# Kernel tuning notes

Hardware: AMD Instinct MI355X
Metric: run time of the kernel (lower is better)

The kernel has to match this reference:

```python
import jax, jax.numpy as jnp
import numpy as np

H = 128
W = 128
DELTA = 7000.0  # sigmainv in the original (delta default 7000)


def setup_inputs() -> dict:
    key = jax.random.key(0)
    k1, k2, k3, k4 = jax.random.split(key, 4)
    B, P, F, TH, TW = 2, 300, 512, 512, 512
    points_bxpx3 = jax.random.uniform(k1, (B, P, 3), jnp.float32) * 2.0 - 1.0  # NDC cube [-1,1]
    faces_fx3 = jax.random.randint(k2, (F, 3), 0, P, dtype=jnp.int32)
    uv_bxpx2 = jax.random.uniform(k3, (B, P, 2), jnp.float32)  # texcoords in [0,1]
    texture_bx3xthxtw = jax.random.uniform(k4, (B, 3, TH, TW), jnp.float32)
    return {"points_bxpx3": points_bxpx3, "faces_fx3": faces_fx3,
            "uv_bxpx2": uv_bxpx2, "texture_bx3xthxtw": texture_bx3xthxtw}


def _edge(ax, ay, bx, by, px, py):
    # signed area * 2 of triangle (a, b, p); standard edge function
    return (bx - ax) * (py - ay) - (by - ay) * (px - ax)


def _seg_d2(ax, ay, bx, by, px, py):
    # squared distance from point p to segment (a, b)
    abx, aby = bx - ax, by - ay
    apx, apy = px - ax, py - ay
    denom = abx * abx + aby * aby + 1e-12
    t = jnp.clip((apx * abx + apy * aby) / denom, 0.0, 1.0)
    dx = apx - t * abx
    dy = apy - t * aby
    return dx * dx + dy * dy


def _rasterize(points_bxpx3, faces_fx3, feats_bxfx3xd, height, width, delta):
    """Soft DIB-R-style rasterizer.
    Returns (imfeat [B,H,W,D], improb [B,H,W,1]).
    """
    B = points_bxpx3.shape[0]
    v = points_bxpx3[:, faces_fx3]                      # (B,F,3,3) gathered face vertices
    x0, x1, x2 = (v[:, :, i, 0][:, :, None, None] for i in range(3))
    y0, y1, y2 = (v[:, :, i, 1][:, :, None, None] for i in range(3))
    z0, z1, z2 = (v[:, :, i, 2][:, :, None, None] for i in range(3))

    # pixel-center grid in NDC; y flipped (top row = +1)
    px = ((jnp.arange(width, dtype=points_bxpx3.dtype) + 0.5) / width * 2.0 - 1.0)[None, None, None, :]
    py = (1.0 - (jnp.arange(height, dtype=points_bxpx3.dtype) + 0.5) / height * 2.0)[None, None, :, None]

    area = _edge(x0, y0, x1, y1, x2, y2)                # (B,F,1,1) == normal_z (cross-product z)
    front = area > 1e-8                                  # front-facing (normalz > 0) cull
    inv_area = 1.0 / jnp.where(front, area, 1.0)

    w0 = _edge(x1, y1, x2, y2, px, py) * inv_area        # (B,F,H,W) barycentrics
    w1 = _edge(x2, y2, x0, y0, px, py) * inv_area
    w2 = _edge(x0, y0, x1, y1, px, py) * inv_area
    inside = front & (w0 >= 0) & (w1 >= 0) & (w2 >= 0)

    z_pix = w0 * z0 + w1 * z1 + w2 * z2                  # interpolated depth
    zbuf = jnp.where(inside, z_pix, -1e9)
    best = jnp.argmax(zbuf, axis=1)                      # (B,H,W) nearest covering face
    hit = jnp.any(inside, axis=1)[..., None].astype(points_bxpx3.dtype)  # (B,H,W,1)

    # gather winning barycentrics and per-face vertex features
    w = jnp.stack([w0, w1, w2], axis=-1)                 # (B,F,H,W,3)
    idx = jnp.broadcast_to(best[:, None, :, :, None], (B, 1, height, width, 3))
    wb = jnp.take_along_axis(w, idx, axis=1)[:, 0]       # (B,H,W,3)
    fb = jax.vmap(lambda f, i: f[i])(feats_bxfx3xd, best)  # (B,H,W,3,D)
    imfeat = jnp.einsum('bhwk,bhwkd->bhwd', wb, fb) * hit

    # soft coverage: prob of each face = exp(-delta * d2(pixel, triangle)); z-buffer blend
    d2 = jnp.minimum(
        jnp.minimum(_seg_d2(x0, y0, x1, y1, px, py), _seg_d2(x1, y1, x2, y2, px, py)),
        _seg_d2(x2, y2, x0, y0, px, py))
    d2 = jnp.where(inside, 0.0, d2)
    p = jnp.where(front, jnp.exp(-delta * d2), 0.0)      # (B,F,H,W)
    log_miss = jnp.sum(jnp.log1p(-jnp.clip(p, 0.0, 1.0 - 1e-7)), axis=1)  # (B,H,W)
    improb = (1.0 - jnp.exp(log_miss))[..., None]
    return imfeat, improb


def _fragmentshader(imtexcoords, texture_bx3xthxtw, hardmask):
    # bilinear texture sampling; background is zero
    B, C, TH, TW = texture_bx3xthxtw.shape
    u = jnp.clip(imtexcoords[..., 0], 0.0, 1.0)
    vv = jnp.clip(imtexcoords[..., 1], 0.0, 1.0)
    fx = u * (TW - 1)
    fy = (1.0 - vv) * (TH - 1)
    x0 = jnp.floor(fx).astype(jnp.int32); x1 = jnp.minimum(x0 + 1, TW - 1)
    y0 = jnp.floor(fy).astype(jnp.int32); y1 = jnp.minimum(y0 + 1, TH - 1)
    wx = (fx - x0)[:, None]; wy = (fy - y0)[:, None]     # (B,1,H,W)

    def g(tex, yy, xx):  # tex (C,TH,TW), yy/xx (H,W) -> (C,H,W)
        return tex[:, yy, xx]
    c00 = jax.vmap(g)(texture_bx3xthxtw, y0, x0)
    c01 = jax.vmap(g)(texture_bx3xthxtw, y0, x1)
    c10 = jax.vmap(g)(texture_bx3xthxtw, y1, x0)
    c11 = jax.vmap(g)(texture_bx3xthxtw, y1, x1)
    col = (c00 * (1 - wx) * (1 - wy) + c01 * wx * (1 - wy)
           + c10 * (1 - wx) * wy + c11 * wx * wy)        # (B,C,H,W)
    return col.transpose(0, 2, 3, 1) * hardmask          # (B,H,W,C)


def reference(points_bxpx3, faces_fx3, uv_bxpx2, texture_bx3xthxtw):
    # texture mode: per-face vertex features = [u, v, mask=1]
    uvf = uv_bxpx2[:, faces_fx3]                          # (B,F,3,2)
    ones = jnp.ones_like(uvf[..., :1])
    feats = jnp.concatenate([uvf, ones], axis=-1)         # (B,F,3,3)
    imfeat, improb = _rasterize(points_bxpx3, faces_fx3, feats, H, W, DELTA)
    imtexcoords = imfeat[..., :2]
    hardmask = jax.lax.stop_gradient(imfeat[..., 2:3])    # .detach() in the original
    imrender = _fragmentshader(imtexcoords, texture_bx3xthxtw, hardmask)
    return imrender, improb
```

## Files before the change

### kernel.cpp

```cpp
#include <hip/hip_runtime.h>
#include <math.h>

constexpr int kB = 2, kP = 300, kF = 512, kH = 128, kW = 128, kTH = 512, kTW = 512;
constexpr float kDelta = 7000.0f;
constexpr float kCut = 0.0363f;
constexpr float kThr2 = 0.012928f;
constexpr float kLogInside = -15.9423847f;

__global__ __launch_bounds__(512, 6) void render_all(const float* __restrict__ pts,
                                                     const int* __restrict__ faces,
                                                     const float* __restrict__ uvs,
                                                     const float* __restrict__ tex,
                                                     float* __restrict__ out) {
    __shared__ float4 sA[kF], sB[kF], sC[kF];
    __shared__ float2 s_vtx[kF * 3];
    __shared__ ushort4 s_j3[kF];
    __shared__ float s_uv[kP * 2];
    __shared__ float s_bz[512];
    __shared__ int s_bi[512];
    __shared__ float s_lm[512];
    __shared__ float4 s_pxW[64];
    __shared__ int4 s_pxO[64];
    __shared__ int s_wsum[8];

    int tile = (int)blockIdx.x;
    int b = tile >> 8;
    int rem = tile & 255;
    int ty = rem >> 4, tx = rem & 15;
    int tid = (int)threadIdx.x;
    int lane = tid & 63;
    int wv = tid >> 6;

    {
        int f = tid;
        int i0 = faces[f * 3 + 0], i1 = faces[f * 3 + 1], i2 = faces[f * 3 + 2];
        const float* pb = pts + b * kP * 3;
        float x0 = pb[i0 * 3], y0 = pb[i0 * 3 + 1], z0 = pb[i0 * 3 + 2];
        float x1 = pb[i1 * 3], y1 = pb[i1 * 3 + 1], z1 = pb[i1 * 3 + 2];
        float x2 = pb[i2 * 3], y2 = pb[i2 * 3 + 1], z2 = pb[i2 * 3 + 2];
        float area = (x1 - x0) * (y2 - y0) - (y1 - y0) * (x2 - x0);
        bool front = area > 1e-8f;

        const float* gu = uvs + b * (kP * 2);
        for (int i = tid; i < kP * 2; i += 512) s_uv[i] = gu[i];
        sA[f] = make_float4(0.0f, 0.0f, -1e30f, 0.0f);
        sB[f] = make_float4(0.0f, -1e30f, 0.0f, 0.0f);
        sC[f] = make_float4(-1e30f, 0.0f, 0.0f, 0.0f);
        s_vtx[f * 3 + 0] = make_float2(1e15f, 1e15f);
        s_vtx[f * 3 + 1] = make_float2(1e15f, 1e15f);
        s_vtx[f * 3 + 2] = make_float2(1e15f, 1e15f);
        unsigned long long bal = __ballot(front);
        if (lane == 0) s_wsum[wv] = __popcll(bal);
        __syncthreads();

        int base = 0;
#pragma unroll
        for (int w = 0; w < 8; ++w) base += (w < wv) ? s_wsum[w] : 0;
        int k = base + __popcll(bal & ((1ull << lane) - 1ull));

        if (front) {
            int slot = ((k & 7) << 6) | (k >> 3);
            float inv_a = 1.0f / area;
            float e0x = x2 - x1, e0y = y2 - y1;
            float e1x = x0 - x2, e1y = y0 - y2;
            float e2x = x1 - x0, e2y = y1 - y0;
            float l0 = fmaf(e0x, e0x, e0y * e0y);
            float l1 = fmaf(e1x, e1x, e1y * e1y);
            float l2 = fmaf(e2x, e2x, e2y * e2y);
            float s0 = rsqrtf(l0 + 1e-12f);
            float s1 = rsqrtf(l1 + 1e-12f);
            float s2 = rsqrtf(l2 + 1e-12f);
            float A0 = -e0y * s0, B0 = e0x * s0, C0 = (e0y * x1 - e0x * y1) * s0;
            float A1 = -e1y * s1, B1 = e1x * s1, C1 = (e1y * x2 - e1x * y2) * s1;
            float A2 = -e2y * s2, B2 = e2x * s2, C2 = (e2y * x0 - e2x * y0) * s2;
            float a0 = -e0y * inv_a, b0 = e0x * inv_a, c0 = (e0y * x1 - e0x * y1) * inv_a;
            float a1 = -e1y * inv_a, b1 = e1x * inv_a, c1 = (e1y * x2 - e1x * y2) * inv_a;
            float a2 = -e2y * inv_a, b2 = e2x * inv_a, c2 = (e2y * x0 - e2x * y0) * inv_a;
            sA[slot] = make_float4(A0, B0, C0, A1);
            sB[slot] = make_float4(B1, C1, A2, B2);
            sC[slot] = make_float4(C2,
                                   a0 * z0 + a1 * z1 + a2 * z2,
                                   b0 * z0 + b1 * z1 + b2 * z2,
                                   c0 * z0 + c1 * z1 + c2 * z2);
            s_vtx[slot * 3 + 0] = make_float2(x0, y0);
            s_vtx[slot * 3 + 1] = make_float2(x1, y1);
            s_vtx[slot * 3 + 2] = make_float2(x2, y2);
            s_j3[slot] = make_ushort4((unsigned short)i0, (unsigned short)i1,
                                      (unsigned short)i2, 0);
        }
    }
    __syncthreads();

    int pyi = ty * 8 + (lane >> 3);
    int pxi = tx * 8 + (lane & 7);
    float px = ((float)pxi + 0.5f) * (2.0f / 128.0f) - 1.0f;
    float py = 1.0f - ((float)pyi + 0.5f) * (2.0f / 128.0f);

    float cx = (float)(tx * 8 + 4) * (2.0f / 128.0f) - 1.0f;
    float cy = 1.0f - (float)(ty * 8 + 4) * (2.0f / 128.0f);
    unsigned long long m;
    {
        int slt = (wv << 6) + lane;
        float4 a4 = sA[slt];
        float4 b4 = sB[slt];
        float4 c4 = sC[slt];
        float L0 = fmaf(a4.x, cx, fmaf(a4.y, cy, a4.z));
        float L1 = fmaf(a4.w, cx, fmaf(b4.x, cy, b4.y));
        float L2 = fmaf(b4.z, cx, fmaf(b4.w, cy, c4.x));
        float minc = fminf(fminf(L0, L1), L2);
        float2 v0 = s_vtx[slt * 3 + 0];
        float2 v1 = s_vtx[slt * 3 + 1];
        float2 v2 = s_vtx[slt * 3 + 2];
        float e0x = v2.x - v1.x, e0y = v2.y - v1.y;
        float e1x = v0.x - v2.x, e1y = v0.y - v2.y;
        float e2x = v1.x - v0.x, e2y = v1.y - v0.y;
        float p0x = cx - v0.x, p0y = cy - v0.y;
        float p1x = cx - v1.x, p1y = cy - v1.y;
        float p2x = cx - v2.x, p2y = cy - v2.y;
        float dot0 = fmaf(p1x, e0x, p1y * e0y), len0 = fmaf(e0x, e0x, e0y * e0y);
        float dot1 = fmaf(p2x, e1x, p2y * e1y), len1 = fmaf(e1x, e1x, e1y * e1y);
        float dot2 = fmaf(p0x, e2x, p0y * e2y), len2 = fmaf(e2x, e2x, e2y * e2y);
        float c0 = (dot0 >= 0.0f && dot0 <= len0) ? L0 * L0 : 1e30f;
        float c1 = (dot1 >= 0.0f && dot1 <= len1) ? L1 * L1 : 1e30f;
        float c2 = (dot2 >= 0.0f && dot2 <= len2) ? L2 * L2 : 1e30f;
        float dv0 = fmaf(p0x, p0x, p0y * p0y);
        float dv1 = fmaf(p1x, p1x, p1y * p1y);
        float dv2 = fmaf(p2x, p2x, p2y * p2y);
        float d2c = fminf(fminf(fminf(c0, c1), fminf(c2, dv0)), fminf(dv1, dv2));
        bool admit = (minc >= 0.0f) | (d2c <= kThr2);
        m = __ballot(admit);
    }

    float bestz = -1e9f;
    int besti = -1, icnt = 0;
    float lm = 0.0f;

    int l = -1;
    float4 h0, h1, h2;
    if (m) {
        l = (int)__builtin_ctzll(m);
        m &= (m - 1);
        int fs = (wv << 6) + l;
        h0 = sA[fs]; h1 = sB[fs]; h2 = sC[fs];
    }
    while (l >= 0) {
        int l2 = -1;
        float4 n0, n1, n2;
        if (m) {
            l2 = (int)__builtin_ctzll(m);
            m &= (m - 1);
            int fs2 = (wv << 6) + l2;
            n0 = sA[fs2]; n1 = sB[fs2]; n2 = sC[fs2];
        }
        int fs = (wv << 6) + l;
        int k = (l << 3) | wv;
        float L0 = fmaf(h0.x, px, fmaf(h0.y, py, h0.z));
        float L1 = fmaf(h0.w, px, fmaf(h1.x, py, h1.y));
        float L2 = fmaf(h1.z, px, fmaf(h1.w, py, h2.x));
        float minL = fminf(fminf(L0, L1), L2);
        bool inside = minL >= 0.0f;
        float z = fmaf(h2.y, px, fmaf(h2.z, py, h2.w));
        if (inside && z > bestz) { bestz = z; besti = k; }
        icnt += inside ? 1 : 0;
        float db = fminf(fminf(fabsf(L0), fabsf(L1)), fabsf(L2));
        bool need = (!inside) & (db < kCut);
        if (__any(need)) {
            float2 v0 = s_vtx[fs * 3 + 0];
            float2 v1 = s_vtx[fs * 3 + 1];
            float2 v2 = s_vtx[fs * 3 + 2];
            float e0x = v2.x - v1.x, e0y = v2.y - v1.y;
            float e1x = v0.x - v2.x, e1y = v0.y - v2.y;
            float e2x = v1.x - v0.x, e2y = v1.y - v0.y;
            float p0x = px - v0.x, p0y = py - v0.y;
            float p1x = px - v1.x, p1y = py - v1.y;
            float p2x = px - v2.x, p2y = py - v2.y;
            float dot0 = fmaf(p1x, e0x, p1y * e0y), len0 = fmaf(e0x, e0x, e0y * e0y);
            float dot1 = fmaf(p2x, e1x, p2y * e1y), len1 = fmaf(e1x, e1x, e1y * e1y);
            float dot2 = fmaf(p0x, e2x, p0y * e2y), len2 = fmaf(e2x, e2x, e2y * e2y);
            float c0 = (dot0 >= 0.0f && dot0 <= len0) ? L0 * L0 : 1e30f;
            float c1 = (dot1 >= 0.0f && dot1 <= len1) ? L1 * L1 : 1e30f;
            float c2 = (dot2 >= 0.0f && dot2 <= len2) ? L2 * L2 : 1e30f;
            float dv0 = fmaf(p0x, p0x, p0y * p0y);
            float dv1 = fmaf(p1x, p1x, p1y * p1y);
            float dv2 = fmaf(p2x, p2x, p2y * p2y);
            float d2 = fminf(fminf(fminf(c0, c1), fminf(c2, dv0)), fminf(dv1, dv2));
            float p = __expf(-kDelta * d2);
            p = fminf(p, 1.0f - 1e-7f);
            float lp = __logf(1.0f - p);
            lm += need ? lp : 0.0f;
        }
        l = l2; h0 = n0; h1 = n1; h2 = n2;
    }
    lm = fmaf((float)icnt, kLogInside, lm);

    s_bz[tid] = bestz;
    s_bi[tid] = besti;
    s_lm[tid] = lm;
    __syncthreads();

    if (tid < 64) {
        float bz = s_bz[tid];
        int bi = s_bi[tid];
        float L = s_lm[tid];
#pragma unroll
        for (int w = 1; w < 8; ++w) {
            float z2 = s_bz[w * 64 + tid];
            int ii = s_bi[w * 64 + tid];
            L += s_lm[w * 64 + tid];
            if (z2 > bz || (z2 == bz && ii >= 0 && (unsigned)ii < (unsigned)bi)) {
                bz = z2; bi = ii;
            }
        }
        float improb = 1.0f - expf(L);
        float u = 0.0f, v = 0.0f, mk = 0.0f;
        if (bi >= 0) {
            int slot = ((bi & 7) << 6) | (bi >> 3);
            float2 v0 = s_vtx[slot * 3 + 0];
            float2 v1 = s_vtx[slot * 3 + 1];
            float2 v2 = s_vtx[slot * 3 + 2];
            float area = (v1.x - v0.x) * (v2.y - v0.y) - (v1.y - v0.y) * (v2.x - v0.x);
            float inv_a = 1.0f / area;
            float w0 = ((v2.x - v1.x) * (py - v1.y) - (v2.y - v1.y) * (px - v1.x)) * inv_a;
            float w1 = ((v0.x - v2.x) * (py - v2.y) - (v0.y - v2.y) * (px - v2.x)) * inv_a;
            float w2 = ((v1.x - v0.x) * (py - v0.y) - (v1.y - v0.y) * (px - v0.x)) * inv_a;
            ushort4 j = s_j3[slot];
            u = w0 * s_uv[j.x * 2] + w1 * s_uv[j.y * 2] + w2 * s_uv[j.z * 2];
            v = w0 * s_uv[j.x * 2 + 1] + w1 * s_uv[j.y * 2 + 1] + w2 * s_uv[j.z * 2 + 1];
            mk = w0 + w1 + w2;
        }
        float uc = fminf(fmaxf(u, 0.0f), 1.0f);
        float vc = fminf(fmaxf(v, 0.0f), 1.0f);
        float fx = uc * (float)(kTW - 1);
        float fy = (1.0f - vc) * (float)(kTH - 1);
        int xi0 = (int)floorf(fx), yi0 = (int)floorf(fy);
        int xi1 = min(xi0 + 1, kTW - 1), yi1 = min(yi0 + 1, kTH - 1);
        float wx = fx - (float)xi0, wy = fy - (float)yi0;
        float w00 = (1.0f - wx) * (1.0f - wy) * mk;
        float w01 = wx * (1.0f - wy) * mk;
        float w10 = (1.0f - wx) * wy * mk;
        float w11 = wx * wy * mk;
        s_pxW[tid] = make_float4(w00, w01, w10, w11);
        s_pxO[tid] = make_int4(yi0 * kTW + xi0, yi0 * kTW + xi1,
                               yi1 * kTW + xi0, yi1 * kTW + xi1);
        out[kB * kH * kW * 3 + (b * kH + pyi) * kW + pxi] = improb;
    }
    __syncthreads();

    if (tid < 192) {
        int pix = tid & 63;
        int c = tid >> 6;
        float4 w = s_pxW[pix];
        int4 o = s_pxO[pix];
        const float* tc = tex + ((size_t)b * 3 + c) * kTH * kTW;
        float col = tc[o.x] * w.x + tc[o.y] * w.y + tc[o.z] * w.z + tc[o.w] * w.w;
        int qy = ty * 8 + (pix >> 3);
        int qx = tx * 8 + (pix & 7);
        out[((b * kH + qy) * kW + qx) * 3 + c] = col;
    }
}

extern "C" void kernel_launch(void* const* d_in, const int* in_sizes, int n_in,
                              void* d_out, int out_size, void* d_ws, size_t ws_size,
                              hipStream_t stream) {
    const float* pts = (const float*)d_in[0];
    const int* faces = (const int*)d_in[1];
    const float* uvs = (const float*)d_in[2];
    const float* tex = (const float*)d_in[3];
    float* out = (float*)d_out;
    render_all<<<kB * 256, 512, 0, stream>>>(pts, faces, uvs, tex, out);
}
```

Before: 18.44 us.

## Process two pixel tiles per block to amortize per-face setup

Each block now renders two adjacent 8x8 tiles in a loop, and the grid is halved, so the shared-memory face setup (gathering vertices, building edge and depth coefficients) runs once per two tiles instead of once per tile. The face loop is also simplified: the software prefetch of the next face's coefficients is dropped in favour of plain per-iteration shared loads. The tradeoff is half as many blocks in flight, which lowers parallelism across the GPU, and the two tiles run one after the other inside each block.

```diff
diff --git a/kernel.cpp b/kernel.cpp
--- a/kernel.cpp
+++ b/kernel.cpp
@@ -23,10 +23,11 @@
     __shared__ int4 s_pxO[64];
     __shared__ int s_wsum[8];
 
-    int tile = (int)blockIdx.x;
-    int b = tile >> 8;
-    int rem = tile & 255;
-    int ty = rem >> 4, tx = rem & 15;
+    int blk = (int)blockIdx.x;
+    int b = blk >> 7;
+    int rem = blk & 127;
+    int ty = rem >> 3;
+    int txp = rem & 7;
     int tid = (int)threadIdx.x;
     int lane = tid & 63;
     int wv = tid >> 6;
@@ -91,89 +92,34 @@
     }
     __syncthreads();
 
-    int pyi = ty * 8 + (lane >> 3);
-    int pxi = tx * 8 + (lane & 7);
-    float px = ((float)pxi + 0.5f) * (2.0f / 128.0f) - 1.0f;
-    float py = 1.0f - ((float)pyi + 0.5f) * (2.0f / 128.0f);
-
-    float cx = (float)(tx * 8 + 4) * (2.0f / 128.0f) - 1.0f;
-    float cy = 1.0f - (float)(ty * 8 + 4) * (2.0f / 128.0f);
-    unsigned long long m;
-    {
-        int slt = (wv << 6) + lane;
-        float4 a4 = sA[slt];
-        float4 b4 = sB[slt];
-        float4 c4 = sC[slt];
-        float L0 = fmaf(a4.x, cx, fmaf(a4.y, cy, a4.z));
-        float L1 = fmaf(a4.w, cx, fmaf(b4.x, cy, b4.y));
-        float L2 = fmaf(b4.z, cx, fmaf(b4.w, cy, c4.x));
-        float minc = fminf(fminf(L0, L1), L2);
-        float2 v0 = s_vtx[slt * 3 + 0];
-        float2 v1 = s_vtx[slt * 3 + 1];
-        float2 v2 = s_vtx[slt * 3 + 2];
-        float e0x = v2.x - v1.x, e0y = v2.y - v1.y;
-        float e1x = v0.x - v2.x, e1y = v0.y - v2.y;
-        float e2x = v1.x - v0.x, e2y = v1.y - v0.y;
-        float p0x = cx - v0.x, p0y = cy - v0.y;
-        float p1x = cx - v1.x, p1y = cy - v1.y;
-        float p2x = cx - v2.x, p2y = cy - v2.y;
-        float dot0 = fmaf(p1x, e0x, p1y * e0y), len0 = fmaf(e0x, e0x, e0y * e0y);
-        float dot1 = fmaf(p2x, e1x, p2y * e1y), len1 = fmaf(e1x, e1x, e1y * e1y);
-        float dot2 = fmaf(p0x, e2x, p0y * e2y), len2 = fmaf(e2x, e2x, e2y * e2y);
-        float c0 = (dot0 >= 0.0f && dot0 <= len0) ? L0 * L0 : 1e30f;
-        float c1 = (dot1 >= 0.0f && dot1 <= len1) ? L1 * L1 : 1e30f;
-        float c2 = (dot2 >= 0.0f && dot2 <= len2) ? L2 * L2 : 1e30f;
-        float dv0 = fmaf(p0x, p0x, p0y * p0y);
-        float dv1 = fmaf(p1x, p1x, p1y * p1y);
-        float dv2 = fmaf(p2x, p2x, p2y * p2y);
-        float d2c = fminf(fminf(fminf(c0, c1), fminf(c2, dv0)), fminf(dv1, dv2));
-        bool admit = (minc >= 0.0f) | (d2c <= kThr2);
-        m = __ballot(admit);
-    }
-
-    float bestz = -1e9f;
-    int besti = -1, icnt = 0;
-    float lm = 0.0f;
-
-    int l = -1;
-    float4 h0, h1, h2;
-    if (m) {
-        l = (int)__builtin_ctzll(m);
-        m &= (m - 1);
-        int fs = (wv << 6) + l;
-        h0 = sA[fs]; h1 = sB[fs]; h2 = sC[fs];
-    }
-    while (l >= 0) {
-        int l2 = -1;
-        float4 n0, n1, n2;
-        if (m) {
-            l2 = (int)__builtin_ctzll(m);
-            m &= (m - 1);
-            int fs2 = (wv << 6) + l2;
-            n0 = sA[fs2]; n1 = sB[fs2]; n2 = sC[fs2];
-        }
-        int fs = (wv << 6) + l;
-        int k = (l << 3) | wv;
-        float L0 = fmaf(h0.x, px, fmaf(h0.y, py, h0.z));
-        float L1 = fmaf(h0.w, px, fmaf(h1.x, py, h1.y));
-        float L2 = fmaf(h1.z, px, fmaf(h1.w, py, h2.x));
-        float minL = fminf(fminf(L0, L1), L2);
-        bool inside = minL >= 0.0f;
-        float z = fmaf(h2.y, px, fmaf(h2.z, py, h2.w));
-        if (inside && z > bestz) { bestz = z; besti = k; }
-        icnt += inside ? 1 : 0;
-        float db = fminf(fminf(fabsf(L0), fabsf(L1)), fabsf(L2));
-        bool need = (!inside) & (db < kCut);
-        if (__any(need)) {
-            float2 v0 = s_vtx[fs * 3 + 0];
-            float2 v1 = s_vtx[fs * 3 + 1];
-            float2 v2 = s_vtx[fs * 3 + 2];
+    for (int it = 0; it < 2; ++it) {
+        int tx = txp * 2 + it;
+        int pyi = ty * 8 + (lane >> 3);
+        int pxi = tx * 8 + (lane & 7);
+        float px = ((float)pxi + 0.5f) * (2.0f / 128.0f) - 1.0f;
+        float py = 1.0f - ((float)pyi + 0.5f) * (2.0f / 128.0f);
+
+        float cx = (float)(tx * 8 + 4) * (2.0f / 128.0f) - 1.0f;
+        float cy = 1.0f - (float)(ty * 8 + 4) * (2.0f / 128.0f);
+        unsigned long long m;
+        {
+            int slt = (wv << 6) + lane;
+            float4 a4 = sA[slt];
+            float4 b4 = sB[slt];
+            float4 c4 = sC[slt];
+            float L0 = fmaf(a4.x, cx, fmaf(a4.y, cy, a4.z));
+            float L1 = fmaf(a4.w, cx, fmaf(b4.x, cy, b4.y));
+            float L2 = fmaf(b4.z, cx, fmaf(b4.w, cy, c4.x));
+            float minc = fminf(fminf(L0, L1), L2);
+            float2 v0 = s_vtx[slt * 3 + 0];
+            float2 v1 = s_vtx[slt * 3 + 1];
+            float2 v2 = s_vtx[slt * 3 + 2];
             float e0x = v2.x - v1.x, e0y = v2.y - v1.y;
             float e1x = v0.x - v2.x, e1y = v0.y - v2.y;
             float e2x = v1.x - v0.x, e2y = v1.y - v0.y;
-            float p0x = px - v0.x, p0y = py - v0.y;
-            float p1x = px - v1.x, p1y = py - v1.y;
-            float p2x = px - v2.x, p2y = py - v2.y;
+            float p0x = cx - v0.x, p0y = cy - v0.y;
+            float p1x = cx - v1.x, p1y = cy - v1.y;
+            float p2x = cx - v2.x, p2y = cy - v2.y;
             float dot0 = fmaf(p1x, e0x, p1y * e0y), len0 = fmaf(e0x, e0x, e0y * e0y);
             float dot1 = fmaf(p2x, e1x, p2y * e1y), len1 = fmaf(e1x, e1x, e1y * e1y);
             float dot2 = fmaf(p0x, e2x, p0y * e2y), len2 = fmaf(e2x, e2x, e2y * e2y);
@@ -183,79 +129,125 @@
             float dv0 = fmaf(p0x, p0x, p0y * p0y);
             float dv1 = fmaf(p1x, p1x, p1y * p1y);
             float dv2 = fmaf(p2x, p2x, p2y * p2y);
-            float d2 = fminf(fminf(fminf(c0, c1), fminf(c2, dv0)), fminf(dv1, dv2));
-            float p = __expf(-kDelta * d2);
-            p = fminf(p, 1.0f - 1e-7f);
-            float lp = __logf(1.0f - p);
-            lm += need ? lp : 0.0f;
-        }
-        l = l2; h0 = n0; h1 = n1; h2 = n2;
-    }
-    lm = fmaf((float)icnt, kLogInside, lm);
-
-    s_bz[tid] = bestz;
-    s_bi[tid] = besti;
-    s_lm[tid] = lm;
-    __syncthreads();
-
-    if (tid < 64) {
-        float bz = s_bz[tid];
-        int bi = s_bi[tid];
-        float L = s_lm[tid];
+            float d2c = fminf(fminf(fminf(c0, c1), fminf(c2, dv0)), fminf(dv1, dv2));
+            bool admit = (minc >= 0.0f) | (d2c <= kThr2);
+            m = __ballot(admit);
+        }
+
+        float bestz = -1e9f;
+        int besti = -1, icnt = 0;
+        float lm = 0.0f;
+
+        while (m) {
+            int l = (int)__builtin_ctzll(m);
+            m &= (m - 1);
+            int fs = (wv << 6) + l;
+            int k = (l << 3) | wv;
+            float4 h0 = sA[fs];
+            float4 h1 = sB[fs];
+            float4 h2 = sC[fs];
+            float L0 = fmaf(h0.x, px, fmaf(h0.y, py, h0.z));
+            float L1 = fmaf(h0.w, px, fmaf(h1.x, py, h1.y));
+            float L2 = fmaf(h1.z, px, fmaf(h1.w, py, h2.x));
+            float minL = fminf(fminf(L0, L1), L2);
+            bool inside = minL >= 0.0f;
+            float z = fmaf(h2.y, px, fmaf(h2.z, py, h2.w));
+            if (inside && z > bestz) { bestz = z; besti = k; }
+            icnt += inside ? 1 : 0;
+            float db = fminf(fminf(fabsf(L0), fabsf(L1)), fabsf(L2));
+            bool need = (!inside) & (db < kCut);
+            if (__any(need)) {
+                float2 v0 = s_vtx[fs * 3 + 0];
+                float2 v1 = s_vtx[fs * 3 + 1];
+                float2 v2 = s_vtx[fs * 3 + 2];
+                float e0x = v2.x - v1.x, e0y = v2.y - v1.y;
+                float e1x = v0.x - v2.x, e1y = v0.y - v2.y;
+                float e2x = v1.x - v0.x, e2y = v1.y - v0.y;
+                float p0x = px - v0.x, p0y = py - v0.y;
+                float p1x = px - v1.x, p1y = py - v1.y;
+                float p2x = px - v2.x, p2y = py - v2.y;
+                float dot0 = fmaf(p1x, e0x, p1y * e0y), len0 = fmaf(e0x, e0x, e0y * e0y);
+                float dot1 = fmaf(p2x, e1x, p2y * e1y), len1 = fmaf(e1x, e1x, e1y * e1y);
+                float dot2 = fmaf(p0x, e2x, p0y * e2y), len2 = fmaf(e2x, e2x, e2y * e2y);
+                float c0 = (dot0 >= 0.0f && dot0 <= len0) ? L0 * L0 : 1e30f;
+                float c1 = (dot1 >= 0.0f && dot1 <= len1) ? L1 * L1 : 1e30f;
+                float c2 = (dot2 >= 0.0f && dot2 <= len2) ? L2 * L2 : 1e30f;
+                float dv0 = fmaf(p0x, p0x, p0y * p0y);
+                float dv1 = fmaf(p1x, p1x, p1y * p1y);
+                float dv2 = fmaf(p2x, p2x, p2y * p2y);
+                float d2 = fminf(fminf(fminf(c0, c1), fminf(c2, dv0)), fminf(dv1, dv2));
+                float p = __expf(-kDelta * d2);
+                p = fminf(p, 1.0f - 1e-7f);
+                float lp = __logf(1.0f - p);
+                lm += need ? lp : 0.0f;
+            }
+        }
+        lm = fmaf((float)icnt, kLogInside, lm);
+
+        s_bz[tid] = bestz;
+        s_bi[tid] = besti;
+        s_lm[tid] = lm;
+        __syncthreads();
+
+        if (tid < 64) {
+            float bz = s_bz[tid];
+            int bi = s_bi[tid];
+            float L = s_lm[tid];
 #pragma unroll
-        for (int w = 1; w < 8; ++w) {
-            float z2 = s_bz[w * 64 + tid];
-            int ii = s_bi[w * 64 + tid];
-            L += s_lm[w * 64 + tid];
-            if (z2 > bz || (z2 == bz && ii >= 0 && (unsigned)ii < (unsigned)bi)) {
-                bz = z2; bi = ii;
+            for (int w = 1; w < 8; ++w) {
+                float z2 = s_bz[w * 64 + tid];
+                int ii = s_bi[w * 64 + tid];
+                L += s_lm[w * 64 + tid];
+                if (z2 > bz || (z2 == bz && ii >= 0 && (unsigned)ii < (unsigned)bi)) {
+                    bz = z2; bi = ii;
+                }
             }
-        }
-        float improb = 1.0f - expf(L);
-        float u = 0.0f, v = 0.0f, mk = 0.0f;
-        if (bi >= 0) {
-            int slot = ((bi & 7) << 6) | (bi >> 3);
-            float2 v0 = s_vtx[slot * 3 + 0];
-            float2 v1 = s_vtx[slot * 3 + 1];
-            float2 v2 = s_vtx[slot * 3 + 2];
-            float area = (v1.x - v0.x) * (v2.y - v0.y) - (v1.y - v0.y) * (v2.x - v0.x);
-            float inv_a = 1.0f / area;
-            float w0 = ((v2.x - v1.x) * (py - v1.y) - (v2.y - v1.y) * (px - v1.x)) * inv_a;
-            float w1 = ((v0.x - v2.x) * (py - v2.y) - (v0.y - v2.y) * (px - v2.x)) * inv_a;
-            float w2 = ((v1.x - v0.x) * (py - v0.y) - (v1.y - v0.y) * (px - v0.x)) * inv_a;
-            ushort4 j = s_j3[slot];
-            u = w0 * s_uv[j.x * 2] + w1 * s_uv[j.y * 2] + w2 * s_uv[j.z * 2];
-            v = w0 * s_uv[j.x * 2 + 1] + w1 * s_uv[j.y * 2 + 1] + w2 * s_uv[j.z * 2 + 1];
-            mk = w0 + w1 + w2;
-        }
-        float uc = fminf(fmaxf(u, 0.0f), 1.0f);
-        float vc = fminf(fmaxf(v, 0.0f), 1.0f);
-        float fx = uc * (float)(kTW - 1);
-        float fy = (1.0f - vc) * (float)(kTH - 1);
-        int xi0 = (int)floorf(fx), yi0 = (int)floorf(fy);
-        int xi1 = min(xi0 + 1, kTW - 1), yi1 = min(yi0 + 1, kTH - 1);
-        float wx = fx - (float)xi0, wy = fy - (float)yi0;
-        float w00 = (1.0f - wx) * (1.0f - wy) * mk;
-        float w01 = wx * (1.0f - wy) * mk;
-        float w10 = (1.0f - wx) * wy * mk;
-        float w11 = wx * wy * mk;
-        s_pxW[tid] = make_float4(w00, w01, w10, w11);
-        s_pxO[tid] = make_int4(yi0 * kTW + xi0, yi0 * kTW + xi1,
-                               yi1 * kTW + xi0, yi1 * kTW + xi1);
-        out[kB * kH * kW * 3 + (b * kH + pyi) * kW + pxi] = improb;
-    }
-    __syncthreads();
-
-    if (tid < 192) {
-        int pix = tid & 63;
-        int c = tid >> 6;
-        float4 w = s_pxW[pix];
-        int4 o = s_pxO[pix];
-        const float* tc = tex + ((size_t)b * 3 + c) * kTH * kTW;
-        float col = tc[o.x] * w.x + tc[o.y] * w.y + tc[o.z] * w.z + tc[o.w] * w.w;
-        int qy = ty * 8 + (pix >> 3);
-        int qx = tx * 8 + (pix & 7);
-        out[((b * kH + qy) * kW + qx) * 3 + c] = col;
+            float improb = 1.0f - expf(L);
+            float u = 0.0f, v = 0.0f, mk = 0.0f;
+            if (bi >= 0) {
+                int slot = ((bi & 7) << 6) | (bi >> 3);
+                float2 v0 = s_vtx[slot * 3 + 0];
+                float2 v1 = s_vtx[slot * 3 + 1];
+                float2 v2 = s_vtx[slot * 3 + 2];
+                float area = (v1.x - v0.x) * (v2.y - v0.y) - (v1.y - v0.y) * (v2.x - v0.x);
+                float inv_a = 1.0f / area;
+                float w0 = ((v2.x - v1.x) * (py - v1.y) - (v2.y - v1.y) * (px - v1.x)) * inv_a;
+                float w1 = ((v0.x - v2.x) * (py - v2.y) - (v0.y - v2.y) * (px - v2.x)) * inv_a;
+                float w2 = ((v1.x - v0.x) * (py - v0.y) - (v1.y - v0.y) * (px - v0.x)) * inv_a;
+                ushort4 j = s_j3[slot];
+                u = w0 * s_uv[j.x * 2] + w1 * s_uv[j.y * 2] + w2 * s_uv[j.z * 2];
+                v = w0 * s_uv[j.x * 2 + 1] + w1 * s_uv[j.y * 2 + 1] + w2 * s_uv[j.z * 2 + 1];
+                mk = w0 + w1 + w2;
+            }
+            float uc = fminf(fmaxf(u, 0.0f), 1.0f);
+            float vc = fminf(fmaxf(v, 0.0f), 1.0f);
+            float fx = uc * (float)(kTW - 1);
+            float fy = (1.0f - vc) * (float)(kTH - 1);
+            int xi0 = (int)floorf(fx), yi0 = (int)floorf(fy);
+            int xi1 = min(xi0 + 1, kTW - 1), yi1 = min(yi0 + 1, kTH - 1);
+            float wx = fx - (float)xi0, wy = fy - (float)yi0;
+            float w00 = (1.0f - wx) * (1.0f - wy) * mk;
+            float w01 = wx * (1.0f - wy) * mk;
+            float w10 = (1.0f - wx) * wy * mk;
+            float w11 = wx * wy * mk;
+            s_pxW[tid] = make_float4(w00, w01, w10, w11);
+            s_pxO[tid] = make_int4(yi0 * kTW + xi0, yi0 * kTW + xi1,
+                                   yi1 * kTW + xi0, yi1 * kTW + xi1);
+            out[kB * kH * kW * 3 + (b * kH + pyi) * kW + pxi] = improb;
+        }
+        __syncthreads();
+
+        if (tid < 192) {
+            int pix = tid & 63;
+            int c = tid >> 6;
+            float4 w = s_pxW[pix];
+            int4 o = s_pxO[pix];
+            const float* tc = tex + ((size_t)b * 3 + c) * kTH * kTW;
+            float col = tc[o.x] * w.x + tc[o.y] * w.y + tc[o.z] * w.z + tc[o.w] * w.w;
+            int qy = ty * 8 + (pix >> 3);
+            int qx = tx * 8 + (pix & 7);
+            out[((b * kH + qy) * kW + qx) * 3 + c] = col;
+        }
     }
 }
 
@@ -267,5 +259,5 @@
     const float* uvs = (const float*)d_in[2];
     const float* tex = (const float*)d_in[3];
     float* out = (float*)d_out;
-    render_all<<<kB * 256, 512, 0, stream>>>(pts, faces, uvs, tex, out);
+    render_all<<<kB * 128, 512, 0, stream>>>(pts, faces, uvs, tex, out);
 }
```

Result: slower. 21.71 us (+17.7%).
